# Kernel optimization log

Hardware: AMD Instinct MI355X
Metric: run time of the kernel (lower is better)

## Reference

```python
import jax, jax.numpy as jnp
import numpy as np

N, E, T = 10000, 50000, 80000   # nodes, edges, triplets
D, H, C, CF = 16, 128, 64, 64   # n_orb, hidden_dim, conv_dim, coeffs_dim


def l2norm(v):
    # matches torch F.normalize(dim=-1): x / max(||x||_2, 1e-12)
    return v / jnp.maximum(jnp.linalg.norm(v, axis=-1, keepdims=True), 1e-12)


def setup_inputs() -> dict:
    key = jax.random.key(0)
    ks = jax.random.split(key, 16)

    def w(k, i, o):
        return jax.random.normal(k, (i, o), jnp.float32) / np.sqrt(i).astype(np.float32)

    return {
        "x": jax.random.normal(ks[0], (N, H), jnp.float32),
        "cji": jax.random.normal(ks[1], (E, D, CF), jnp.float32),
        "robs": jax.random.normal(ks[2], (E, D), jnp.float32),
        "shbs": jax.random.normal(ks[3], (T, D), jnp.float32),
        "idx_i": jax.random.randint(ks[4], (E,), 0, N),
        "idx_j": jax.random.randint(ks[5], (E,), 0, N),
        "tri_idx_k": jax.random.randint(ks[6], (T,), 0, N),
        "edge_idx_kj": jax.random.randint(ks[7], (T,), 0, E),
        "edge_idx_ji": jax.random.randint(ks[8], (T,), 0, E),
        "W_nb": w(ks[9], H, 2 * C), "b_nb": jnp.zeros((2 * C,), jnp.float32),
        "W_c1": w(ks[10], CF, C),
        "W_c2": w(ks[11], C, 2 * C),
        "W_t3": w(ks[12], C, C), "b_t3": jnp.zeros((C,), jnp.float32),
        "W_n1": w(ks[13], 2 * C, C), "b_n1": jnp.zeros((C,), jnp.float32),
        "W_n2": w(ks[14], C, C), "b_n2": jnp.zeros((C,), jnp.float32),
        "W_na": w(ks[15], C, H),
    }


def reference(x, cji, robs, shbs, idx_i, idx_j, tri_idx_k, edge_idx_kj,
              edge_idx_ji, W_nb, b_nb, W_c1, W_c2, W_t3, b_t3, W_n1, b_n1,
              W_n2, b_n2, W_na):
    silu = jax.nn.silu
    # node_before_lin + chunk
    h = x @ W_nb + b_nb                       # [N, 2C]
    xq, xk = jnp.split(h, 2, axis=-1)         # each [N, C]
    # coeffs_before_lin: act -> Dense -> act -> Dense (no biases)
    c = silu(silu(cji) @ W_c1) @ W_c2         # [E, D, 2C]
    cji2, ckj = jnp.split(c, 2, axis=-1)      # each [E, D, C]
    # triplet gathers
    ckj_g = l2norm(ckj[edge_idx_kj])          # [T, D, C]
    tbo = l2norm(jnp.einsum('td,tdh->th', shbs * robs[edge_idx_kj], ckj_g))  # [T, C]
    tbw = tbo * jax.nn.sigmoid(xk[tri_idx_k])  # [T, C]
    # scatter triplets -> edges (dim_size = robs.size(0) = E)
    agg = jax.ops.segment_sum(tbw, edge_idx_ji, num_segments=E)  # [E, C]
    tbw2 = silu(agg) @ W_t3 + b_t3            # three_lin, [E, C]
    cji3 = l2norm(cji2 * (1.0 + tbw2[:, None, :]))  # cji + cji*w, normalized
    lcao = l2norm(jnp.einsum('ed,edh->eh', robs, cji3))  # [E, C]
    # node message: node_lin on concatenated endpoint features
    m = jnp.concatenate([xq[idx_i], xq[idx_j]], axis=-1)  # [E, 2C]
    m = silu(silu(m) @ W_n1 + b_n1) @ W_n2 + b_n2          # [E, C]
    out = x + jax.ops.segment_sum(lcao * m, idx_i, num_segments=N) @ W_na
    return out
```

## Files before the change

### kernel.cpp

```cpp
#include <hip/hip_runtime.h>
#include <hip/hip_bf16.h>

#define NN 10000
#define EE 50000
#define TT 80000
#define DD 16
#define HH 128
#define CC 64

typedef __hip_bfloat16 bf16;
typedef __attribute__((ext_vector_type(8))) short bf16x8;
typedef __attribute__((ext_vector_type(4))) short bf16x4;
typedef __attribute__((ext_vector_type(4))) float f32x4;

__device__ __forceinline__ float silu_f(float x) {
  return x * __builtin_amdgcn_rcpf(1.f + __expf(-x));
}
__device__ __forceinline__ float sigm_f(float x) {
  return __builtin_amdgcn_rcpf(1.f + __expf(-x));
}

__device__ __forceinline__ short f2bs(float x) {
  __hip_bfloat16 h = __float2bfloat16(x);
  short s;
  __builtin_memcpy(&s, &h, 2);
  return s;
}

__device__ __forceinline__ float rnorm_f(float ss) {
  return __builtin_amdgcn_rcpf(fmaxf(__builtin_amdgcn_sqrtf(ss), 1e-12f));
}

__device__ __forceinline__ void bf2x(unsigned u, float& lo, float& hi) {
  lo = __uint_as_float(u << 16);
  hi = __uint_as_float(u & 0xffff0000u);
}

#define ZERO_U4 960000
__global__ __launch_bounds__(256) void k_zero(uint4* __restrict__ p) {
  const int stride = gridDim.x * 256;
  for (int i = blockIdx.x * 256 + threadIdx.x; i < ZERO_U4; i += stride)
    p[i] = (uint4){0u, 0u, 0u, 0u};
}

__global__ __launch_bounds__(128) void k_node(
    const float* __restrict__ x, const float* __restrict__ W_nb,
    const float* __restrict__ b_nb, float* __restrict__ sxq,
    float* __restrict__ sigxk) {
  __shared__ __align__(16) float xs[8][HH];
  const int t = threadIdx.x;
  const int base = blockIdx.x * 8;
#pragma unroll
  for (int i = 0; i < 8; ++i) xs[i][t] = x[(size_t)(base + i) * HH + t];
  __syncthreads();
  float acc[8];
  const float bb = b_nb[t];
#pragma unroll
  for (int i = 0; i < 8; ++i) acc[i] = bb;
  for (int k = 0; k < HH; k += 4) {
    const float w0 = W_nb[(k + 0) * HH + t];
    const float w1 = W_nb[(k + 1) * HH + t];
    const float w2 = W_nb[(k + 2) * HH + t];
    const float w3 = W_nb[(k + 3) * HH + t];
#pragma unroll
    for (int i = 0; i < 8; ++i) {
      const float4 xv = *(const float4*)(&xs[i][k]);
      acc[i] = fmaf(xv.x, w0, acc[i]);
      acc[i] = fmaf(xv.y, w1, acc[i]);
      acc[i] = fmaf(xv.z, w2, acc[i]);
      acc[i] = fmaf(xv.w, w3, acc[i]);
    }
  }
  if (t < CC) {
#pragma unroll
    for (int i = 0; i < 8; ++i)
      sxq[(size_t)(base + i) * CC + t] = silu_f(acc[i]);
  } else {
#pragma unroll
    for (int i = 0; i < 8; ++i)
      sigxk[(size_t)(base + i) * CC + (t - CC)] = sigm_f(acc[i]);
  }
}

#define K2_BLOCKS 2048
#define K2_TILES 50000
__global__ __launch_bounds__(256, 2) void k_coeffs(
    const float* __restrict__ cji, const float* __restrict__ W_c1,
    const float* __restrict__ W_c2, bf16* __restrict__ cji2,
    bf16* __restrict__ ckjn) {
  const int tid = threadIdx.x;
  const int w = tid >> 6, l = tid & 63;
  const int lr = l & 15, lg = l >> 4;

  bf16x4 bw1[4][4];
  bf16x4 bw2[4][8];
#pragma unroll
  for (int rt = 0; rt < 4; ++rt)
#pragma unroll
    for (int kt = 0; kt < 4; ++kt) {
      bf16x4 t;
#pragma unroll
      for (int b = 0; b < 4; ++b)
        t[b] = f2bs(W_c1[(kt * 16 + lg * 4 + b) * 64 + rt * 16 + lr]);
      bw1[rt][kt] = t;
    }
#pragma unroll
  for (int kt = 0; kt < 4; ++kt)
#pragma unroll
    for (int ct = 0; ct < 8; ++ct) {
      bf16x4 t;
#pragma unroll
      for (int b = 0; b < 4; ++b)
        t[b] = f2bs(W_c2[(kt * 16 + lg * 4 + b) * 128 + ct * 16 + lr]);
      bw2[kt][ct] = t;
    }

  const int nwave = K2_BLOCKS * 4;
  int tile = blockIdx.x * 4 + w;
  if (tile >= K2_TILES) return;

  float4 r[4];
#pragma unroll
  for (int kt = 0; kt < 4; ++kt)
    r[kt] = *(const float4*)(cji + (size_t)tile * 1024 + lr * 64 + kt * 16 + lg * 4);

  for (; tile < K2_TILES; tile += nwave) {
    bf16x4 sB[4];
#pragma unroll
    for (int kt = 0; kt < 4; ++kt) {
      bf16x4 t;
      t[0] = f2bs(silu_f(r[kt].x));
      t[1] = f2bs(silu_f(r[kt].y));
      t[2] = f2bs(silu_f(r[kt].z));
      t[3] = f2bs(silu_f(r[kt].w));
      sB[kt] = t;
    }

    const int next = tile + nwave;
    if (next < K2_TILES) {
#pragma unroll
      for (int kt = 0; kt < 4; ++kt)
        r[kt] = *(const float4*)(cji + (size_t)next * 1024 + lr * 64 + kt * 16 + lg * 4);
    }

    f32x4 acc1[4];
#pragma unroll
    for (int rt = 0; rt < 4; ++rt) acc1[rt] = (f32x4){0.f, 0.f, 0.f, 0.f};
#pragma unroll
    for (int rt = 0; rt < 4; ++rt)
#pragma unroll
      for (int kt = 0; kt < 4; ++kt)
        acc1[rt] = __builtin_amdgcn_mfma_f32_16x16x16bf16_1k(bw1[rt][kt], sB[kt], acc1[rt], 0, 0, 0);

    bf16x4 tf[4];
#pragma unroll
    for (int kt = 0; kt < 4; ++kt) {
      bf16x4 t;
#pragma unroll
      for (int b = 0; b < 4; ++b) t[b] = f2bs(silu_f(acc1[kt][b]));
      tf[kt] = t;
    }

    f32x4 acc2[8];
#pragma unroll
    for (int ct = 0; ct < 8; ++ct) acc2[ct] = (f32x4){0.f, 0.f, 0.f, 0.f};
#pragma unroll
    for (int ct = 0; ct < 8; ++ct)
#pragma unroll
      for (int kt = 0; kt < 4; ++kt)
        acc2[ct] = __builtin_amdgcn_mfma_f32_16x16x16bf16_1k(tf[kt], bw2[kt][ct], acc2[ct], 0, 0, 0);

    float rn[4];
#pragma unroll
    for (int j = 0; j < 4; ++j) {
      float ss = acc2[4][j] * acc2[4][j];
      ss = fmaf(acc2[5][j], acc2[5][j], ss);
      ss = fmaf(acc2[6][j], acc2[6][j], ss);
      ss = fmaf(acc2[7][j], acc2[7][j], ss);
#pragma unroll
      for (int m = 1; m < 16; m <<= 1) ss += __shfl_xor(ss, m, 64);
      rn[j] = rnorm_f(ss);
    }

    union { short h[16]; uint4 u[2]; } p;
#pragma unroll
    for (int ct = 0; ct < 4; ++ct)
#pragma unroll
      for (int j = 0; j < 4; ++j) p.h[ct * 4 + j] = f2bs(acc2[ct][j]);
    {
      uint4* d0 = (uint4*)(cji2 + (size_t)tile * 1024 + l * 16);
      d0[0] = p.u[0];
      d0[1] = p.u[1];
    }
#pragma unroll
    for (int ct = 0; ct < 4; ++ct)
#pragma unroll
      for (int j = 0; j < 4; ++j) p.h[ct * 4 + j] = f2bs(acc2[4 + ct][j] * rn[j]);
    {
      uint4* d1 = (uint4*)(ckjn + (size_t)tile * 1024 + l * 16);
      d1[0] = p.u[0];
      d1[1] = p.u[1];
    }
  }
}

#define K3_WAVES 20000
__global__ __launch_bounds__(256) void k_triplet(
    const bf16* __restrict__ ckjn, const float* __restrict__ shbs,
    const float* __restrict__ robs, const float* __restrict__ sigxk,
    const int* __restrict__ tri_idx_k, const int* __restrict__ edge_idx_kj,
    const int* __restrict__ edge_idx_ji, float* __restrict__ agg) {
  const int wid = (blockIdx.x * 256 + threadIdx.x) >> 6;
  const int l = threadIdx.x & 63;
  if (wid >= K3_WAVES) return;
  const int lq = l >> 4;
  const int t0 = wid * 4;

  int kj[4], kn[4], ji[4];
#pragma unroll
  for (int i = 0; i < 4; ++i) {
    kj[i] = edge_idx_kj[t0 + i];
    kn[i] = tri_idx_k[t0 + i];
    ji[i] = edge_idx_ji[t0 + i];
  }
  float4 sh[4], rb[4];
  uint4 u0[4], u1[4];
  float sx[4];
#pragma unroll
  for (int i = 0; i < 4; ++i) {
    sh[i] = *(const float4*)(shbs + (size_t)(t0 + i) * DD + lq * 4);
    rb[i] = *(const float4*)(robs + (size_t)kj[i] * DD + lq * 4);
    const uint4* b = (const uint4*)(ckjn + (size_t)kj[i] * 1024 + l * 16);
    u0[i] = b[0];
    u1[i] = b[1];
    sx[i] = sigxk[(size_t)kn[i] * CC + l];
  }

  float acc[4][4];
#pragma unroll
  for (int i = 0; i < 4; ++i) {
    const float w0 = sh[i].x * rb[i].x, w1 = sh[i].y * rb[i].y,
                w2 = sh[i].z * rb[i].z, w3 = sh[i].w * rb[i].w;
    float x0, x1, x2, x3;
    bf2x(u0[i].x, x0, x1); bf2x(u0[i].y, x2, x3);
    acc[i][0] = fmaf(w3, x3, fmaf(w2, x2, fmaf(w1, x1, w0 * x0)));
    bf2x(u0[i].z, x0, x1); bf2x(u0[i].w, x2, x3);
    acc[i][1] = fmaf(w3, x3, fmaf(w2, x2, fmaf(w1, x1, w0 * x0)));
    bf2x(u1[i].x, x0, x1); bf2x(u1[i].y, x2, x3);
    acc[i][2] = fmaf(w3, x3, fmaf(w2, x2, fmaf(w1, x1, w0 * x0)));
    bf2x(u1[i].z, x0, x1); bf2x(u1[i].w, x2, x3);
    acc[i][3] = fmaf(w3, x3, fmaf(w2, x2, fmaf(w1, x1, w0 * x0)));
  }
#pragma unroll
  for (int m = 16; m < 64; m <<= 1)
#pragma unroll
    for (int i = 0; i < 4; ++i)
#pragma unroll
      for (int q = 0; q < 4; ++q) acc[i][q] += __shfl_xor(acc[i][q], m, 64);

  float sel[4], ss[4];
#pragma unroll
  for (int i = 0; i < 4; ++i) {
    sel[i] = (lq == 0) ? acc[i][0] : (lq == 1) ? acc[i][1]
             : (lq == 2) ? acc[i][2] : acc[i][3];
    ss[i] = sel[i] * sel[i];
  }
#pragma unroll
  for (int m = 1; m < 64; m <<= 1)
#pragma unroll
    for (int i = 0; i < 4; ++i) ss[i] += __shfl_xor(ss[i], m, 64);
#pragma unroll
  for (int i = 0; i < 4; ++i) {
    const float tbw = sel[i] * rnorm_f(ss[i]) * sx[i];
    atomicAdd(&agg[(size_t)ji[i] * CC + l], tbw);
  }
}

#define K4A_TILES 3125
#define K4A_BLOCKS 256
__global__ __launch_bounds__(256, 2) void k_edge_a(
    const float* __restrict__ agg, const float* __restrict__ sxq,
    const int* __restrict__ idx_i, const int* __restrict__ idx_j,
    const float* __restrict__ W_t3, const float* __restrict__ b_t3,
    const float* __restrict__ W_n1, const float* __restrict__ b_n1,
    const float* __restrict__ W_n2, const float* __restrict__ b_n2,
    float* __restrict__ onew_buf, float* __restrict__ m_buf) {
  __shared__ __align__(16) float fbuf[4][16 * 68];
  __shared__ __align__(16) short sbuf[4][16 * 72];
  const int tid = threadIdx.x;
  const int w = tid >> 6, l = tid & 63;
  const int lr = l & 15, lg = l >> 4;
  float* fb = fbuf[w];
  short* sb = sbuf[w];

  bf16x8 bt3[2][4], bn1[4][4], bn2[2][4];
#pragma unroll
  for (int kt = 0; kt < 2; ++kt)
#pragma unroll
    for (int nt = 0; nt < 4; ++nt) {
      bf16x8 t;
#pragma unroll
      for (int b = 0; b < 8; ++b)
        t[b] = f2bs(W_t3[(kt * 32 + lg * 8 + b) * 64 + nt * 16 + lr]);
      bt3[kt][nt] = t;
    }
#pragma unroll
  for (int kt = 0; kt < 4; ++kt)
#pragma unroll
    for (int nt = 0; nt < 4; ++nt) {
      bf16x8 t;
#pragma unroll
      for (int b = 0; b < 8; ++b)
        t[b] = f2bs(W_n1[(kt * 32 + lg * 8 + b) * 64 + nt * 16 + lr]);
      bn1[kt][nt] = t;
    }
#pragma unroll
  for (int kt = 0; kt < 2; ++kt)
#pragma unroll
    for (int nt = 0; nt < 4; ++nt) {
      bf16x8 t;
#pragma unroll
      for (int b = 0; b < 8; ++b)
        t[b] = f2bs(W_n2[(kt * 32 + lg * 8 + b) * 64 + nt * 16 + lr]);
      bn2[kt][nt] = t;
    }
  float bt3c[4], bn1c[4], bn2c[4];
#pragma unroll
  for (int nt = 0; nt < 4; ++nt) {
    bt3c[nt] = b_t3[nt * 16 + lr];
    bn1c[nt] = b_n1[nt * 16 + lr];
    bn2c[nt] = b_n2[nt * 16 + lr];
  }

  for (int tile = blockIdx.x * 4 + w; tile < K4A_TILES; tile += K4A_BLOCKS * 4) {
    const int e = tile * 16 + lr;
    const int vi = idx_i[e], vj = idx_j[e];

    bf16x8 aagg[2];
#pragma unroll
    for (int kt = 0; kt < 2; ++kt) {
      const float4 u = *(const float4*)(agg + (size_t)e * 64 + kt * 32 + lg * 8);
      const float4 v = *(const float4*)(agg + (size_t)e * 64 + kt * 32 + lg * 8 + 4);
      bf16x8 t;
      t[0] = f2bs(silu_f(u.x)); t[1] = f2bs(silu_f(u.y));
      t[2] = f2bs(silu_f(u.z)); t[3] = f2bs(silu_f(u.w));
      t[4] = f2bs(silu_f(v.x)); t[5] = f2bs(silu_f(v.y));
      t[6] = f2bs(silu_f(v.z)); t[7] = f2bs(silu_f(v.w));
      aagg[kt] = t;
    }
    f32x4 acc[4];
#pragma unroll
    for (int nt = 0; nt < 4; ++nt) acc[nt] = (f32x4){0.f, 0.f, 0.f, 0.f};
#pragma unroll
    for (int nt = 0; nt < 4; ++nt) {
      acc[nt] = __builtin_amdgcn_mfma_f32_16x16x32_bf16(aagg[0], bt3[0][nt], acc[nt], 0, 0, 0);
      acc[nt] = __builtin_amdgcn_mfma_f32_16x16x32_bf16(aagg[1], bt3[1][nt], acc[nt], 0, 0, 0);
    }
#pragma unroll
    for (int nt = 0; nt < 4; ++nt)
#pragma unroll
      for (int j = 0; j < 4; ++j)
        fb[(lg * 4 + j) * 68 + nt * 16 + lr] = 1.f + bt3c[nt] + acc[nt][j];
    {
      const int row = l >> 2, cs = (l & 3) * 16;
      float* dst = onew_buf + (size_t)(tile * 16 + row) * 64 + cs;
#pragma unroll
      for (int q = 0; q < 4; ++q)
        *(float4*)(dst + q * 4) = *(const float4*)(fb + row * 68 + cs + q * 4);
    }

    bf16x8 am[4];
#pragma unroll
    for (int kt = 0; kt < 4; ++kt) {
      const float* src = (kt < 2) ? (sxq + (size_t)vi * 64 + kt * 32)
                                  : (sxq + (size_t)vj * 64 + (kt - 2) * 32);
      const float4 u = *(const float4*)(src + lg * 8);
      const float4 v = *(const float4*)(src + lg * 8 + 4);
      bf16x8 t;
      t[0] = f2bs(u.x); t[1] = f2bs(u.y); t[2] = f2bs(u.z); t[3] = f2bs(u.w);
      t[4] = f2bs(v.x); t[5] = f2bs(v.y); t[6] = f2bs(v.z); t[7] = f2bs(v.w);
      am[kt] = t;
    }
    f32x4 acc1[4];
#pragma unroll
    for (int nt = 0; nt < 4; ++nt) acc1[nt] = (f32x4){0.f, 0.f, 0.f, 0.f};
#pragma unroll
    for (int nt = 0; nt < 4; ++nt)
#pragma unroll
      for (int kt = 0; kt < 4; ++kt)
        acc1[nt] = __builtin_amdgcn_mfma_f32_16x16x32_bf16(am[kt], bn1[kt][nt], acc1[nt], 0, 0, 0);

#pragma unroll
    for (int nt = 0; nt < 4; ++nt)
#pragma unroll
      for (int j = 0; j < 4; ++j)
        sb[(lg * 4 + j) * 72 + nt * 16 + lr] = f2bs(silu_f(acc1[nt][j] + bn1c[nt]));
    const bf16x8 a20 = *(const bf16x8*)(sb + lr * 72 + lg * 8);
    const bf16x8 a21 = *(const bf16x8*)(sb + lr * 72 + 32 + lg * 8);

    f32x4 acc2[4];
#pragma unroll
    for (int nt = 0; nt < 4; ++nt) acc2[nt] = (f32x4){0.f, 0.f, 0.f, 0.f};
#pragma unroll
    for (int nt = 0; nt < 4; ++nt) {
      acc2[nt] = __builtin_amdgcn_mfma_f32_16x16x32_bf16(a20, bn2[0][nt], acc2[nt], 0, 0, 0);
      acc2[nt] = __builtin_amdgcn_mfma_f32_16x16x32_bf16(a21, bn2[1][nt], acc2[nt], 0, 0, 0);
    }
#pragma unroll
    for (int nt = 0; nt < 4; ++nt)
#pragma unroll
      for (int j = 0; j < 4; ++j)
        fb[(lg * 4 + j) * 68 + nt * 16 + lr] = acc2[nt][j] + bn2c[nt];
    {
      const int row = l >> 2, cs = (l & 3) * 16;
      float* dst = m_buf + (size_t)(tile * 16 + row) * 64 + cs;
#pragma unroll
      for (int q = 0; q < 4; ++q)
        *(float4*)(dst + q * 4) = *(const float4*)(fb + row * 68 + cs + q * 4);
    }
  }
}

#define K4B_WAVES 25000
__global__ __launch_bounds__(256) void k_edge_b(
    const bf16* __restrict__ cji2, const float* __restrict__ robs,
    const float* __restrict__ onew_buf, const float* __restrict__ m_buf,
    const int* __restrict__ idx_i, float* __restrict__ lacc) {
  const int wid = (blockIdx.x * 256 + threadIdx.x) >> 6;
  const int l = threadIdx.x & 63;
  if (wid >= K4B_WAVES) return;
  const int lq = l >> 4, lr = l & 15;
  const int e0 = wid * 2;

  uint4 u0[2], u1[2];
  float4 rb[2];
  float ow[2][4], mm[2];
  int vi[2];
#pragma unroll
  for (int i = 0; i < 2; ++i) {
    const uint4* base = (const uint4*)(cji2 + (size_t)(e0 + i) * 1024 + l * 16);
    u0[i] = base[0];
    u1[i] = base[1];
    const float* ob = onew_buf + (size_t)(e0 + i) * 64 + lr;
    ow[i][0] = ob[0]; ow[i][1] = ob[16]; ow[i][2] = ob[32]; ow[i][3] = ob[48];
    rb[i] = *(const float4*)(robs + (size_t)(e0 + i) * DD + lq * 4);
    mm[i] = m_buf[(size_t)(e0 + i) * 64 + l];
    vi[i] = idx_i[e0 + i];
  }

  float v[2][16];
#pragma unroll
  for (int i = 0; i < 2; ++i) {
    bf2x(u0[i].x, v[i][0], v[i][1]);   bf2x(u0[i].y, v[i][2], v[i][3]);
    bf2x(u0[i].z, v[i][4], v[i][5]);   bf2x(u0[i].w, v[i][6], v[i][7]);
    bf2x(u1[i].x, v[i][8], v[i][9]);   bf2x(u1[i].y, v[i][10], v[i][11]);
    bf2x(u1[i].z, v[i][12], v[i][13]); bf2x(u1[i].w, v[i][14], v[i][15]);
#pragma unroll
    for (int j = 0; j < 4; ++j) {
      v[i][j] *= ow[i][0];
      v[i][4 + j] *= ow[i][1];
      v[i][8 + j] *= ow[i][2];
      v[i][12 + j] *= ow[i][3];
    }
  }
  float sq[2][4];
#pragma unroll
  for (int i = 0; i < 2; ++i)
#pragma unroll
    for (int j = 0; j < 4; ++j)
      sq[i][j] = fmaf(v[i][j], v[i][j],
                 fmaf(v[i][4 + j], v[i][4 + j],
                 fmaf(v[i][8 + j], v[i][8 + j], v[i][12 + j] * v[i][12 + j])));
#pragma unroll
  for (int m = 1; m < 16; m <<= 1)
#pragma unroll
    for (int i = 0; i < 2; ++i)
#pragma unroll
      for (int j = 0; j < 4; ++j) sq[i][j] += __shfl_xor(sq[i][j], m, 64);

  float lcq[2][4];
#pragma unroll
  for (int i = 0; i < 2; ++i) {
    const float t0 = rb[i].x * rnorm_f(sq[i][0]),
                t1 = rb[i].y * rnorm_f(sq[i][1]),
                t2 = rb[i].z * rnorm_f(sq[i][2]),
                t3 = rb[i].w * rnorm_f(sq[i][3]);
#pragma unroll
    for (int q = 0; q < 4; ++q)
      lcq[i][q] = fmaf(t0, v[i][q * 4 + 0],
                  fmaf(t1, v[i][q * 4 + 1],
                  fmaf(t2, v[i][q * 4 + 2], t3 * v[i][q * 4 + 3])));
  }
#pragma unroll
  for (int m = 16; m < 64; m <<= 1)
#pragma unroll
    for (int i = 0; i < 2; ++i)
#pragma unroll
      for (int q = 0; q < 4; ++q) lcq[i][q] += __shfl_xor(lcq[i][q], m, 64);

  float sel[2], ss[2];
#pragma unroll
  for (int i = 0; i < 2; ++i) {
    sel[i] = (lq == 0) ? lcq[i][0] : (lq == 1) ? lcq[i][1]
             : (lq == 2) ? lcq[i][2] : lcq[i][3];
    ss[i] = sel[i] * sel[i];
  }
#pragma unroll
  for (int m = 1; m < 64; m <<= 1)
#pragma unroll
    for (int i = 0; i < 2; ++i) ss[i] += __shfl_xor(ss[i], m, 64);
#pragma unroll
  for (int i = 0; i < 2; ++i) {
    const float lcao = sel[i] * rnorm_f(ss[i]);
    atomicAdd(&lacc[(size_t)vi[i] * CC + l], lcao * mm[i]);
  }
}

__global__ __launch_bounds__(128) void k_out(
    const float* __restrict__ x, const float* __restrict__ lacc,
    const float* __restrict__ W_na, float* __restrict__ out) {
  __shared__ __align__(16) float ls[8][CC];
  const int t = threadIdx.x;
  const int base = blockIdx.x * 8;
  for (int idx = t; idx < 8 * CC; idx += 128)
    ls[idx >> 6][idx & 63] = lacc[(size_t)(base + (idx >> 6)) * CC + (idx & 63)];
  __syncthreads();
  float acc[8];
#pragma unroll
  for (int i = 0; i < 8; ++i) acc[i] = x[(size_t)(base + i) * HH + t];
  for (int k = 0; k < CC; k += 4) {
    const float w0 = W_na[(k + 0) * HH + t];
    const float w1 = W_na[(k + 1) * HH + t];
    const float w2 = W_na[(k + 2) * HH + t];
    const float w3 = W_na[(k + 3) * HH + t];
#pragma unroll
    for (int i = 0; i < 8; ++i) {
      const float4 lv = *(const float4*)(&ls[i][k]);
      acc[i] = fmaf(lv.x, w0, acc[i]);
      acc[i] = fmaf(lv.y, w1, acc[i]);
      acc[i] = fmaf(lv.z, w2, acc[i]);
      acc[i] = fmaf(lv.w, w3, acc[i]);
    }
  }
#pragma unroll
  for (int i = 0; i < 8; ++i) out[(size_t)(base + i) * HH + t] = acc[i];
}

extern "C" void kernel_launch(void* const* d_in, const int* in_sizes, int n_in,
                              void* d_out, int out_size, void* d_ws,
                              size_t ws_size, hipStream_t stream) {
  const float* x = (const float*)d_in[0];
  const float* cji = (const float*)d_in[1];
  const float* robs = (const float*)d_in[2];
  const float* shbs = (const float*)d_in[3];
  const int* idx_i = (const int*)d_in[4];
  const int* idx_j = (const int*)d_in[5];
  const int* tri_idx_k = (const int*)d_in[6];
  const int* edge_idx_kj = (const int*)d_in[7];
  const int* edge_idx_ji = (const int*)d_in[8];
  const float* W_nb = (const float*)d_in[9];
  const float* b_nb = (const float*)d_in[10];
  const float* W_c1 = (const float*)d_in[11];
  const float* W_c2 = (const float*)d_in[12];
  const float* W_t3 = (const float*)d_in[13];
  const float* b_t3 = (const float*)d_in[14];
  const float* W_n1 = (const float*)d_in[15];
  const float* b_n1 = (const float*)d_in[16];
  const float* W_n2 = (const float*)d_in[17];
  const float* b_n2 = (const float*)d_in[18];
  const float* W_na = (const float*)d_in[19];
  float* out = (float*)d_out;

  char* ws = (char*)d_ws;
  const size_t NC4 = (size_t)NN * CC * 4;
  const size_t EDC2 = (size_t)EE * DD * CC * 2;
  const size_t EC4 = (size_t)EE * CC * 4;
  float* sxq = (float*)(ws);
  float* sigxk = (float*)(ws + NC4);
  bf16* cji2 = (bf16*)(ws + 2 * NC4);
  bf16* ckjn = (bf16*)(ws + 2 * NC4 + EDC2);
  float* agg = (float*)(ws + 2 * NC4 + 2 * EDC2);
  float* lacc = (float*)(ws + 2 * NC4 + 2 * EDC2 + EC4);
  float* onew_buf = (float*)(ws + 2 * NC4 + EDC2);
  float* m_buf = (float*)(ws + 2 * NC4 + EDC2 + EC4);

  k_zero<<<1024, 256, 0, stream>>>((uint4*)agg);

  k_node<<<NN / 8, 128, 0, stream>>>(x, W_nb, b_nb, sxq, sigxk);
  k_coeffs<<<K2_BLOCKS, 256, 0, stream>>>(cji, W_c1, W_c2, cji2, ckjn);
  k_triplet<<<(K3_WAVES + 3) / 4, 256, 0, stream>>>(ckjn, shbs, robs, sigxk,
                                                    tri_idx_k, edge_idx_kj,
                                                    edge_idx_ji, agg);
  k_edge_a<<<K4A_BLOCKS, 256, 0, stream>>>(
      agg, sxq, idx_i, idx_j, W_t3, b_t3, W_n1, b_n1, W_n2, b_n2, onew_buf,
      m_buf);
  k_edge_b<<<(K4B_WAVES + 3) / 4, 256, 0, stream>>>(cji2, robs, onew_buf,
                                                    m_buf, idx_i, lacc);
  k_out<<<NN / 8, 128, 0, stream>>>(x, lacc, W_na, out);
}
```

Before: 201.5 us.

## Fold zeroing into node kernel and double-buffer cji prefetch in coeffs kernel

Removes the separate zeroing kernel launch by having k_node clear the agg/lacc workspace alongside its own work. In k_coeffs, cji tiles are now prefetched two iterations ahead using two register buffers, which deepens load latency hiding. The second matmul is split into two halves, which reduces the number of live accumulators. The trade-off is higher register pressure from the extra prefetch buffer and extra store traffic inside k_node.

```diff
diff --git a/kernel.cpp b/kernel.cpp
--- a/kernel.cpp
+++ b/kernel.cpp
@@ -37,21 +37,18 @@
 }
 
 #define ZERO_U4 960000
-__global__ __launch_bounds__(256) void k_zero(uint4* __restrict__ p) {
-  const int stride = gridDim.x * 256;
-  for (int i = blockIdx.x * 256 + threadIdx.x; i < ZERO_U4; i += stride)
-    p[i] = (uint4){0u, 0u, 0u, 0u};
-}
 
 __global__ __launch_bounds__(128) void k_node(
     const float* __restrict__ x, const float* __restrict__ W_nb,
     const float* __restrict__ b_nb, float* __restrict__ sxq,
-    float* __restrict__ sigxk) {
+    float* __restrict__ sigxk, uint4* __restrict__ zero_p) {
   __shared__ __align__(16) float xs[8][HH];
   const int t = threadIdx.x;
   const int base = blockIdx.x * 8;
 #pragma unroll
   for (int i = 0; i < 8; ++i) xs[i][t] = x[(size_t)(base + i) * HH + t];
+  for (int i = blockIdx.x * 128 + t; i < ZERO_U4; i += (NN / 8) * 128)
+    zero_p[i] = (uint4){0u, 0u, 0u, 0u};
   __syncthreads();
   float acc[8];
   const float bb = b_nb[t];
@@ -116,15 +113,20 @@
     }
 
   const int nwave = K2_BLOCKS * 4;
-  int tile = blockIdx.x * 4 + w;
-  if (tile >= K2_TILES) return;
-
-  float4 r[4];
+  const int t0 = blockIdx.x * 4 + w;
+  if (t0 >= K2_TILES) return;
+  const int lane_off = lr * 64 + lg * 4;
+
+  float4 rA[4], rB[4];
 #pragma unroll
   for (int kt = 0; kt < 4; ++kt)
-    r[kt] = *(const float4*)(cji + (size_t)tile * 1024 + lr * 64 + kt * 16 + lg * 4);
-
-  for (; tile < K2_TILES; tile += nwave) {
+    rA[kt] = *(const float4*)(cji + (size_t)t0 * 1024 + lane_off + kt * 16);
+  if (t0 + nwave < K2_TILES)
+#pragma unroll
+    for (int kt = 0; kt < 4; ++kt)
+      rB[kt] = *(const float4*)(cji + (size_t)(t0 + nwave) * 1024 + lane_off + kt * 16);
+
+  auto process = [&](int tile, float4 (&r)[4], int pref_tile) {
     bf16x4 sB[4];
 #pragma unroll
     for (int kt = 0; kt < 4; ++kt) {
@@ -135,12 +137,10 @@
       t[3] = f2bs(silu_f(r[kt].w));
       sB[kt] = t;
     }
-
-    const int next = tile + nwave;
-    if (next < K2_TILES) {
+    if (pref_tile < K2_TILES) {
 #pragma unroll
       for (int kt = 0; kt < 4; ++kt)
-        r[kt] = *(const float4*)(cji + (size_t)next * 1024 + lr * 64 + kt * 16 + lg * 4);
+        r[kt] = *(const float4*)(cji + (size_t)pref_tile * 1024 + lane_off + kt * 16);
     }
 
     f32x4 acc1[4];
@@ -161,46 +161,60 @@
       tf[kt] = t;
     }
 
-    f32x4 acc2[8];
-#pragma unroll
-    for (int ct = 0; ct < 8; ++ct) acc2[ct] = (f32x4){0.f, 0.f, 0.f, 0.f};
-#pragma unroll
-    for (int ct = 0; ct < 8; ++ct)
-#pragma unroll
-      for (int kt = 0; kt < 4; ++kt)
-        acc2[ct] = __builtin_amdgcn_mfma_f32_16x16x16bf16_1k(tf[kt], bw2[kt][ct], acc2[ct], 0, 0, 0);
-
-    float rn[4];
-#pragma unroll
-    for (int j = 0; j < 4; ++j) {
-      float ss = acc2[4][j] * acc2[4][j];
-      ss = fmaf(acc2[5][j], acc2[5][j], ss);
-      ss = fmaf(acc2[6][j], acc2[6][j], ss);
-      ss = fmaf(acc2[7][j], acc2[7][j], ss);
-#pragma unroll
-      for (int m = 1; m < 16; m <<= 1) ss += __shfl_xor(ss, m, 64);
-      rn[j] = rnorm_f(ss);
-    }
-
-    union { short h[16]; uint4 u[2]; } p;
-#pragma unroll
-    for (int ct = 0; ct < 4; ++ct)
-#pragma unroll
-      for (int j = 0; j < 4; ++j) p.h[ct * 4 + j] = f2bs(acc2[ct][j]);
     {
+      f32x4 acc[4];
+#pragma unroll
+      for (int ct = 0; ct < 4; ++ct) acc[ct] = (f32x4){0.f, 0.f, 0.f, 0.f};
+#pragma unroll
+      for (int ct = 0; ct < 4; ++ct)
+#pragma unroll
+        for (int kt = 0; kt < 4; ++kt)
+          acc[ct] = __builtin_amdgcn_mfma_f32_16x16x16bf16_1k(tf[kt], bw2[kt][ct], acc[ct], 0, 0, 0);
+      union { short h[16]; uint4 u[2]; } pa;
+#pragma unroll
+      for (int ct = 0; ct < 4; ++ct)
+#pragma unroll
+        for (int j = 0; j < 4; ++j) pa.h[ct * 4 + j] = f2bs(acc[ct][j]);
       uint4* d0 = (uint4*)(cji2 + (size_t)tile * 1024 + l * 16);
-      d0[0] = p.u[0];
-      d0[1] = p.u[1];
-    }
-#pragma unroll
-    for (int ct = 0; ct < 4; ++ct)
-#pragma unroll
-      for (int j = 0; j < 4; ++j) p.h[ct * 4 + j] = f2bs(acc2[4 + ct][j] * rn[j]);
+      d0[0] = pa.u[0];
+      d0[1] = pa.u[1];
+    }
+
     {
+      f32x4 acc[4];
+#pragma unroll
+      for (int ct = 0; ct < 4; ++ct) acc[ct] = (f32x4){0.f, 0.f, 0.f, 0.f};
+#pragma unroll
+      for (int ct = 0; ct < 4; ++ct)
+#pragma unroll
+        for (int kt = 0; kt < 4; ++kt)
+          acc[ct] = __builtin_amdgcn_mfma_f32_16x16x16bf16_1k(tf[kt], bw2[kt][4 + ct], acc[ct], 0, 0, 0);
+      float rn[4];
+#pragma unroll
+      for (int j = 0; j < 4; ++j) {
+        float ss = acc[0][j] * acc[0][j];
+        ss = fmaf(acc[1][j], acc[1][j], ss);
+        ss = fmaf(acc[2][j], acc[2][j], ss);
+        ss = fmaf(acc[3][j], acc[3][j], ss);
+#pragma unroll
+        for (int m = 1; m < 16; m <<= 1) ss += __shfl_xor(ss, m, 64);
+        rn[j] = rnorm_f(ss);
+      }
+      union { short h[16]; uint4 u[2]; } pb;
+#pragma unroll
+      for (int ct = 0; ct < 4; ++ct)
+#pragma unroll
+        for (int j = 0; j < 4; ++j) pb.h[ct * 4 + j] = f2bs(acc[ct][j] * rn[j]);
       uint4* d1 = (uint4*)(ckjn + (size_t)tile * 1024 + l * 16);
-      d1[0] = p.u[0];
-      d1[1] = p.u[1];
-    }
+      d1[0] = pb.u[0];
+      d1[1] = pb.u[1];
+    }
+  };
+
+  for (int tile = t0; tile < K2_TILES; tile += 2 * nwave) {
+    process(tile, rA, tile + 2 * nwave);
+    if (tile + nwave < K2_TILES)
+      process(tile + nwave, rB, tile + 3 * nwave);
   }
 }
 
@@ -584,9 +598,7 @@
   float* onew_buf = (float*)(ws + 2 * NC4 + EDC2);
   float* m_buf = (float*)(ws + 2 * NC4 + EDC2 + EC4);
 
-  k_zero<<<1024, 256, 0, stream>>>((uint4*)agg);
-
-  k_node<<<NN / 8, 128, 0, stream>>>(x, W_nb, b_nb, sxq, sigxk);
+  k_node<<<NN / 8, 128, 0, stream>>>(x, W_nb, b_nb, sxq, sigxk, (uint4*)agg);
   k_coeffs<<<K2_BLOCKS, 256, 0, stream>>>(cji, W_c1, W_c2, cji2, ckjn);
   k_triplet<<<(K3_WAVES + 3) / 4, 256, 0, stream>>>(ckjn, shbs, robs, sigxk,
                                                     tri_idx_k, edge_idx_kj,
```

New measurement: 194.0 us. -3.7%, faster.

## Fuse zeroing and node projection into coeffs kernel; raise MFMA wave priority

Applied to the files above, without the earlier changes.

Folds the workspace-zeroing kernel and the node linear layer into the coeffs kernel. The first 625 blocks each compute 16 node rows before starting their coeff tiles, which removes two kernel launches and their serialization. It also wraps the MFMA loops in s_setprio to favor matrix issue. The cost is extra LDS, a block-level barrier and load imbalance in the early blocks of the fused kernel.

```diff
diff --git a/kernel.cpp b/kernel.cpp
--- a/kernel.cpp
+++ b/kernel.cpp
@@ -37,60 +37,60 @@
 }
 
 #define ZERO_U4 960000
-__global__ __launch_bounds__(256) void k_zero(uint4* __restrict__ p) {
-  const int stride = gridDim.x * 256;
-  for (int i = blockIdx.x * 256 + threadIdx.x; i < ZERO_U4; i += stride)
-    p[i] = (uint4){0u, 0u, 0u, 0u};
-}
-
-__global__ __launch_bounds__(128) void k_node(
-    const float* __restrict__ x, const float* __restrict__ W_nb,
-    const float* __restrict__ b_nb, float* __restrict__ sxq,
-    float* __restrict__ sigxk) {
-  __shared__ __align__(16) float xs[8][HH];
-  const int t = threadIdx.x;
-  const int base = blockIdx.x * 8;
-#pragma unroll
-  for (int i = 0; i < 8; ++i) xs[i][t] = x[(size_t)(base + i) * HH + t];
-  __syncthreads();
-  float acc[8];
-  const float bb = b_nb[t];
-#pragma unroll
-  for (int i = 0; i < 8; ++i) acc[i] = bb;
-  for (int k = 0; k < HH; k += 4) {
-    const float w0 = W_nb[(k + 0) * HH + t];
-    const float w1 = W_nb[(k + 1) * HH + t];
-    const float w2 = W_nb[(k + 2) * HH + t];
-    const float w3 = W_nb[(k + 3) * HH + t];
-#pragma unroll
-    for (int i = 0; i < 8; ++i) {
-      const float4 xv = *(const float4*)(&xs[i][k]);
-      acc[i] = fmaf(xv.x, w0, acc[i]);
-      acc[i] = fmaf(xv.y, w1, acc[i]);
-      acc[i] = fmaf(xv.z, w2, acc[i]);
-      acc[i] = fmaf(xv.w, w3, acc[i]);
-    }
-  }
-  if (t < CC) {
-#pragma unroll
-    for (int i = 0; i < 8; ++i)
-      sxq[(size_t)(base + i) * CC + t] = silu_f(acc[i]);
-  } else {
-#pragma unroll
-    for (int i = 0; i < 8; ++i)
-      sigxk[(size_t)(base + i) * CC + (t - CC)] = sigm_f(acc[i]);
-  }
-}
 
 #define K2_BLOCKS 2048
 #define K2_TILES 50000
 __global__ __launch_bounds__(256, 2) void k_coeffs(
     const float* __restrict__ cji, const float* __restrict__ W_c1,
     const float* __restrict__ W_c2, bf16* __restrict__ cji2,
-    bf16* __restrict__ ckjn) {
+    bf16* __restrict__ ckjn, const float* __restrict__ x,
+    const float* __restrict__ W_nb, const float* __restrict__ b_nb,
+    float* __restrict__ sxq, float* __restrict__ sigxk,
+    uint4* __restrict__ zero_p) {
+  __shared__ __align__(16) float xs[16][HH];
   const int tid = threadIdx.x;
+  const int bid = blockIdx.x;
   const int w = tid >> 6, l = tid & 63;
   const int lr = l & 15, lg = l >> 4;
+
+  for (int i = bid * 256 + tid; i < ZERO_U4; i += K2_BLOCKS * 256)
+    zero_p[i] = (uint4){0u, 0u, 0u, 0u};
+
+  if (bid < NN / 16) {
+    const int g = tid >> 7, c = tid & 127;
+    const int nb = bid * 16 + g * 8;
+#pragma unroll
+    for (int i = 0; i < 8; ++i)
+      xs[g * 8 + i][c] = x[(size_t)(nb + i) * HH + c];
+    __syncthreads();
+    float acc[8];
+    const float bb = b_nb[c];
+#pragma unroll
+    for (int i = 0; i < 8; ++i) acc[i] = bb;
+    for (int k = 0; k < HH; k += 4) {
+      const float w0 = W_nb[(k + 0) * HH + c];
+      const float w1 = W_nb[(k + 1) * HH + c];
+      const float w2 = W_nb[(k + 2) * HH + c];
+      const float w3 = W_nb[(k + 3) * HH + c];
+#pragma unroll
+      for (int i = 0; i < 8; ++i) {
+        const float4 xv = *(const float4*)(&xs[g * 8 + i][k]);
+        acc[i] = fmaf(xv.x, w0, acc[i]);
+        acc[i] = fmaf(xv.y, w1, acc[i]);
+        acc[i] = fmaf(xv.z, w2, acc[i]);
+        acc[i] = fmaf(xv.w, w3, acc[i]);
+      }
+    }
+    if (c < CC) {
+#pragma unroll
+      for (int i = 0; i < 8; ++i)
+        sxq[(size_t)(nb + i) * CC + c] = silu_f(acc[i]);
+    } else {
+#pragma unroll
+      for (int i = 0; i < 8; ++i)
+        sigxk[(size_t)(nb + i) * CC + (c - CC)] = sigm_f(acc[i]);
+    }
+  }
 
   bf16x4 bw1[4][4];
   bf16x4 bw2[4][8];
@@ -116,7 +116,7 @@
     }
 
   const int nwave = K2_BLOCKS * 4;
-  int tile = blockIdx.x * 4 + w;
+  int tile = bid * 4 + w;
   if (tile >= K2_TILES) return;
 
   float4 r[4];
@@ -146,11 +146,13 @@
     f32x4 acc1[4];
 #pragma unroll
     for (int rt = 0; rt < 4; ++rt) acc1[rt] = (f32x4){0.f, 0.f, 0.f, 0.f};
+    __builtin_amdgcn_s_setprio(1);
 #pragma unroll
     for (int rt = 0; rt < 4; ++rt)
 #pragma unroll
       for (int kt = 0; kt < 4; ++kt)
         acc1[rt] = __builtin_amdgcn_mfma_f32_16x16x16bf16_1k(bw1[rt][kt], sB[kt], acc1[rt], 0, 0, 0);
+    __builtin_amdgcn_s_setprio(0);
 
     bf16x4 tf[4];
 #pragma unroll
@@ -164,11 +166,13 @@
     f32x4 acc2[8];
 #pragma unroll
     for (int ct = 0; ct < 8; ++ct) acc2[ct] = (f32x4){0.f, 0.f, 0.f, 0.f};
+    __builtin_amdgcn_s_setprio(1);
 #pragma unroll
     for (int ct = 0; ct < 8; ++ct)
 #pragma unroll
       for (int kt = 0; kt < 4; ++kt)
         acc2[ct] = __builtin_amdgcn_mfma_f32_16x16x16bf16_1k(tf[kt], bw2[kt][ct], acc2[ct], 0, 0, 0);
+    __builtin_amdgcn_s_setprio(0);
 
     float rn[4];
 #pragma unroll
@@ -584,10 +588,9 @@
   float* onew_buf = (float*)(ws + 2 * NC4 + EDC2);
   float* m_buf = (float*)(ws + 2 * NC4 + EDC2 + EC4);
 
-  k_zero<<<1024, 256, 0, stream>>>((uint4*)agg);
-
-  k_node<<<NN / 8, 128, 0, stream>>>(x, W_nb, b_nb, sxq, sigxk);
-  k_coeffs<<<K2_BLOCKS, 256, 0, stream>>>(cji, W_c1, W_c2, cji2, ckjn);
+  k_coeffs<<<K2_BLOCKS, 256, 0, stream>>>(cji, W_c1, W_c2, cji2, ckjn, x,
+                                          W_nb, b_nb, sxq, sigxk,
+                                          (uint4*)agg);
   k_triplet<<<(K3_WAVES + 3) / 4, 256, 0, stream>>>(ckjn, shbs, robs, sigxk,
                                                     tri_idx_k, edge_idx_kj,
                                                     edge_idx_ji, agg);
```

New measurement: 194.1 us. 3.7% less time.
